# Optimization experiments

Measured on AMD Instinct MI355X. Metric: run time of the kernel, lower is better.

The kernel has to match this reference:

```python
import jax, jax.numpy as jnp
import numpy as np

NUM_HEADS = 12
NUM_PATCHES = 4096
DIM = 768
IN_DIMS = DIM // NUM_HEADS
SCALE = NUM_PATCHES ** (-0.5)
LN_EPS = 1e-5


def setup_inputs() -> dict:
    key = jax.random.key(0)
    ks = jax.random.split(key, 14)
    s = 0.02
    return {
        "x": jax.random.normal(ks[0], (16, NUM_PATCHES, DIM), dtype=jnp.float32),
        "wq": jax.random.normal(ks[1], (DIM, DIM), dtype=jnp.float32) * s,
        "bq": jnp.zeros((DIM,), dtype=jnp.float32),
        "wk": jax.random.normal(ks[2], (DIM, DIM), dtype=jnp.float32) * s,
        "bk": jnp.zeros((DIM,), dtype=jnp.float32),
        "w_g": jax.random.normal(ks[3], (NUM_PATCHES,), dtype=jnp.float32),
        "w_fc": jax.random.normal(ks[4], (IN_DIMS, DIM), dtype=jnp.float32) * s,
        "b_fc": jnp.zeros((DIM,), dtype=jnp.float32),
        "w_fc2": jax.random.normal(ks[5], (NUM_HEADS, NUM_HEADS), dtype=jnp.float32) * s,
        "b_fc2": jnp.zeros((NUM_HEADS,), dtype=jnp.float32),
        "w_proj": jax.random.normal(ks[6], (DIM, DIM), dtype=jnp.float32) * s,
        "b_proj": jnp.zeros((DIM,), dtype=jnp.float32),
        "gamma": jnp.ones((DIM,), dtype=jnp.float32),
        "beta": jnp.zeros((DIM,), dtype=jnp.float32),
    }


def layernorm(x, gamma, beta):
    mu = jnp.mean(x, axis=-1, keepdims=True)
    var = jnp.mean(jnp.square(x - mu), axis=-1, keepdims=True)
    return (x - mu) * jax.lax.rsqrt(var + LN_EPS) * gamma + beta


def reference(x, wq, bq, wk, bk, w_g, w_fc, b_fc, w_fc2, b_fc2, w_proj, b_proj, gamma, beta):
    bs, n, d = x.shape
    q = x @ wq + bq                      # (b,n,d)  fc_q
    k = x @ wk + bk                      # (b,n,d)  fc_k (reassigned x in torch)
    # query_weight = (q^T @ w_g)^T -> (b,1,d); softmax over channel dim
    qw = jnp.einsum("bnd,n->bd", q, w_g) * SCALE
    A = jax.nn.softmax(qw, axis=-1)      # (b,d)
    # G = sum_n(A * k): A is constant over n, so equals A * sum_n k
    G = A * jnp.sum(k, axis=1)           # (b,d)
    # sigmoid gating chain on pooled q
    dv = jnp.mean(q, axis=1)             # (b,d)   AdaptiveAvgPool over n
    dv = dv.reshape(bs, NUM_HEADS, IN_DIMS)
    dv = jax.nn.gelu(dv @ w_fc + b_fc, approximate=False)   # (b,H,d)
    dv = dv.reshape(bs, d, NUM_HEADS)    # reshape (not transpose), as in torch
    dv = dv @ w_fc2 + b_fc2              # (b,d,H)
    dv = jax.nn.sigmoid(jnp.mean(dv, axis=-1))               # (b,d)
    G = G * dv                           # (b,d)
    out = (G[:, None, :] * k) @ w_proj + b_proj + layernorm(k, gamma, beta)
    return out
```

## Files before the change

kernel.cpp:

```cpp
#include <hip/hip_runtime.h>
#include <hip/hip_bf16.h>
#include <math.h>

#define NB 16
#define NP 4096
#define DDIM 768
#define MTOT (NB*NP)
#define N1 1536
#define SCALEF 0.015625f
#define LNEPS 1e-5f

typedef __attribute__((ext_vector_type(8))) short bf16x8;
typedef __attribute__((ext_vector_type(4))) float f32x4;
typedef __attribute__((ext_vector_type(4))) unsigned int u32x4;
typedef unsigned short us;

__device__ __forceinline__ us f2b(float f){
  union { float f; unsigned int u; } v; v.f = f;
  unsigned int u = v.u;
  unsigned int r = (u + 0x7FFFu + ((u >> 16) & 1u)) >> 16;
  return (us)r;
}
__device__ __forceinline__ unsigned int pack2(float a, float b){
  return (unsigned int)f2b(a) | ((unsigned int)f2b(b) << 16);
}
__device__ __forceinline__ float b2f(us h){
  union { unsigned int u; float f; } v; v.u = ((unsigned int)h) << 16;
  return v.f;
}
__device__ __forceinline__ float b2f_lo(unsigned int u){
  union { unsigned int x; float f; } v; v.x = u << 16; return v.f;
}
__device__ __forceinline__ float b2f_hi(unsigned int u){
  union { unsigned int x; float f; } v; v.x = u & 0xFFFF0000u; return v.f;
}

typedef __attribute__((address_space(1))) const unsigned int gas_u32;
typedef __attribute__((address_space(3))) unsigned int las_u32;
__device__ __forceinline__ void gl2lds16(const void* g, void* l){
  __builtin_amdgcn_global_load_lds((gas_u32*)g, (las_u32*)l, 16, 0, 0);
}

__global__ __launch_bounds__(256) void convert_x(const float* __restrict__ x,
                                                 us* __restrict__ xb){
  size_t i = ((size_t)blockIdx.x * 256 + threadIdx.x) * 8;
  const float4* s = reinterpret_cast<const float4*>(x + i);
  float4 a = s[0], b = s[1];
  u32x4 w;
  w[0] = pack2(a.x, a.y); w[1] = pack2(a.z, a.w);
  w[2] = pack2(b.x, b.y); w[3] = pack2(b.z, b.w);
  *reinterpret_cast<u32x4*>(xb + i) = w;
}

__global__ __launch_bounds__(256) void prep_w(const float* __restrict__ wq,
                                              const float* __restrict__ wk,
                                              const float* __restrict__ wp,
                                              us* __restrict__ wt1,
                                              us* __restrict__ wt2){
  int idx = blockIdx.x * 256 + threadIdx.x;
  const int tot1 = N1 * DDIM;
  if (idx < tot1){
    int n = idx / DDIM, k = idx % DDIM;
    float v = (n < DDIM) ? wq[k * DDIM + n] : wk[k * DDIM + (n - DDIM)];
    wt1[idx] = f2b(v);
  }
  int idx2 = idx - tot1;
  if (idx2 >= 0 && idx2 < DDIM * DDIM){
    int n = idx2 / DDIM, k = idx2 % DDIM;
    wt2[idx2] = f2b(wp[k * DDIM + n]);
  }
}

__global__ __launch_bounds__(256) void prep_wb(const us* __restrict__ wt2,
                                               const float* __restrict__ g,
                                               us* __restrict__ wbuf){
  size_t idx = (size_t)blockIdx.x * 256 + threadIdx.x;
  int d = (int)(idx % DDIM);
  size_t nd = idx / DDIM;
  int n = (int)(nd % DDIM);
  int b = (int)(nd / DDIM);
  float v = b2f(wt2[n * DDIM + d]) * g[(size_t)b * DDIM + d];
  wbuf[idx] = f2b(v);
}

__global__ __launch_bounds__(256) void ln_reduce(const float* __restrict__ lnS,
                                                 const float* __restrict__ lnQ,
                                                 float2* __restrict__ rstats){
  int r = blockIdx.x * 256 + threadIdx.x;
  float s = lnS[r] + lnS[MTOT + r] + lnS[2*MTOT + r];
  float q = lnQ[r] + lnQ[MTOT + r] + lnQ[2*MTOT + r];
  float mu = s * (1.0f / DDIM);
  float var = q * (1.0f / DDIM) - mu * mu;
  rstats[r] = make_float2(mu, rsqrtf(var + LNEPS));
}

__device__ __forceinline__ void gemm256_core(const us* __restrict__ Ag,
                                             const us* __restrict__ Bg,
                                             us* lds, int t,
                                             f32x4 (&acc)[4][4][2]){
  us* ldsA = lds;
  us* ldsB = lds + 32768;
  const int wave = t >> 6, lane = t & 63;
  const int wr = wave >> 2, wc = wave & 3, lr = lane & 15, lh = lane >> 4;
  const int srow = t >> 3;
  const int scell = (t & 7) ^ ((t >> 3) & 7);
  const int key8 = lane & 7;

  auto stage_all = [&](int kt){
    int pb = (kt & 1) << 14;
    #pragma unroll
    for (int j = 0; j < 4; ++j){
      const us* sa = Ag + (size_t)(j*64 + srow) * DDIM + kt*64 + scell*8;
      gl2lds16(sa, ldsA + pb + j*4096 + (wave << 9));
    }
    #pragma unroll
    for (int j = 0; j < 4; ++j){
      const us* sb = Bg + (size_t)(j*64 + srow) * DDIM + kt*64 + scell*8;
      gl2lds16(sb, ldsB + pb + j*4096 + (wave << 9));
    }
  };

  stage_all(0);

  bf16x8 av[4][2], bv0[2][2], bv1[2][2];

  for (int kt = 0; kt < 12; ++kt){
    asm volatile("s_waitcnt vmcnt(0)" ::: "memory");
    __builtin_amdgcn_sched_barrier(0);
    __builtin_amdgcn_s_barrier();
    if (kt < 11) stage_all(kt + 1);

    const int pb = (kt & 1) << 14;
    const us* Ab = ldsA + pb;
    const us* Bb = ldsB + pb;

    #pragma unroll
    for (int fm = 0; fm < 4; ++fm){
      int ra = 0*128 + wr*64 + fm*16 + lr;
      #pragma unroll
      for (int kk = 0; kk < 2; ++kk)
        av[fm][kk] = *reinterpret_cast<const bf16x8*>(
            &Ab[ra*64 + ((((kk<<2)|lh) ^ key8) << 3)]);
    }
    #pragma unroll
    for (int fn = 0; fn < 2; ++fn){
      int rb0 = 0*128 + wc*32 + fn*16 + lr;
      int rb1 = 1*128 + wc*32 + fn*16 + lr;
      #pragma unroll
      for (int kk = 0; kk < 2; ++kk){
        bv0[fn][kk] = *reinterpret_cast<const bf16x8*>(
            &Bb[rb0*64 + ((((kk<<2)|lh) ^ key8) << 3)]);
        bv1[fn][kk] = *reinterpret_cast<const bf16x8*>(
            &Bb[rb1*64 + ((((kk<<2)|lh) ^ key8) << 3)]);
      }
    }
    #pragma unroll
    for (int fm = 0; fm < 4; ++fm)
      #pragma unroll
      for (int fn = 0; fn < 2; ++fn)
        #pragma unroll
        for (int kk = 0; kk < 2; ++kk){
          acc[0][fm][fn] = __builtin_amdgcn_mfma_f32_16x16x32_bf16(
              bv0[fn][kk], av[fm][kk], acc[0][fm][fn], 0, 0, 0);
          acc[1][fm][fn] = __builtin_amdgcn_mfma_f32_16x16x32_bf16(
              bv1[fn][kk], av[fm][kk], acc[1][fm][fn], 0, 0, 0);
        }

    #pragma unroll
    for (int fm = 0; fm < 4; ++fm){
      int ra = 1*128 + wr*64 + fm*16 + lr;
      #pragma unroll
      for (int kk = 0; kk < 2; ++kk)
        av[fm][kk] = *reinterpret_cast<const bf16x8*>(
            &Ab[ra*64 + ((((kk<<2)|lh) ^ key8) << 3)]);
    }
    #pragma unroll
    for (int fm = 0; fm < 4; ++fm)
      #pragma unroll
      for (int fn = 0; fn < 2; ++fn)
        #pragma unroll
        for (int kk = 0; kk < 2; ++kk){
          acc[2][fm][fn] = __builtin_amdgcn_mfma_f32_16x16x32_bf16(
              bv0[fn][kk], av[fm][kk], acc[2][fm][fn], 0, 0, 0);
          acc[3][fm][fn] = __builtin_amdgcn_mfma_f32_16x16x32_bf16(
              bv1[fn][kk], av[fm][kk], acc[3][fm][fn], 0, 0, 0);
        }
  }
  __builtin_amdgcn_s_barrier();
}

__global__ __launch_bounds__(512, 2) void gemm_qk(
    const us* __restrict__ xb, const us* __restrict__ wt1,
    const float* __restrict__ bq, const float* __restrict__ bk,
    const float* __restrict__ w_g,
    us* __restrict__ kout,
    float* __restrict__ qwp, float* __restrict__ qsp, float* __restrict__ ksp,
    float* __restrict__ lnS, float* __restrict__ lnQ)
{
  extern __shared__ us lds[];
  int bid = blockIdx.x;
  int swz = (bid & 7) * ((int)gridDim.x >> 3) + (bid >> 3);
  int bn = swz % 6, bm = swz / 6;
  int m0 = bm * 256, n0 = bn * 256;
  int t = threadIdx.x;

  f32x4 acc[4][4][2] = {};
  gemm256_core(xb + (size_t)m0 * DDIM, wt1 + (size_t)n0 * DDIM, lds, t, acc);

  int wave = t >> 6, lane = t & 63;
  int wr = wave >> 2, wc = wave & 3, lr = lane & 15, lh = lane >> 4;
  bool is_q = (n0 < DDIM);
  int b = m0 >> 12, mc = (m0 & (NP-1)) >> 8;

  float4 bias4[2][2];
  #pragma unroll
  for (int qn = 0; qn < 2; ++qn)
    #pragma unroll
    for (int fn = 0; fn < 2; ++fn){
      int col = qn*128 + wc*32 + fn*16 + lh*4;
      bias4[qn][fn] = *reinterpret_cast<const float4*>(
          is_q ? &bq[n0 + col] : &bk[n0 - DDIM + col]);
    }

  #pragma unroll
  for (int p = 0; p < 4; ++p){
    int qm = p >> 1, qn = p & 1;
    #pragma unroll
    for (int fm = 0; fm < 4; ++fm){
      int row = qm*128 + wr*64 + fm*16 + lr;
      #pragma unroll
      for (int fn = 0; fn < 2; ++fn){
        int col = qn*128 + wc*32 + fn*16 + lh*4;
        uint2 w;
        w.x = pack2(acc[p][fm][fn][0] + bias4[qn][fn].x,
                    acc[p][fm][fn][1] + bias4[qn][fn].y);
        w.y = pack2(acc[p][fm][fn][2] + bias4[qn][fn].z,
                    acc[p][fm][fn][3] + bias4[qn][fn].w);
        *reinterpret_cast<uint2*>(&lds[row*256 + (col ^ ((row & 7) << 3))]) = w;
      }
    }
  }
  __syncthreads();

  int c8 = t & 31, rb = t >> 5;
  float cp[8] = {0,0,0,0,0,0,0,0};
  float cpw[8] = {0,0,0,0,0,0,0,0};
  float rs16[16], rq16[16];
  #pragma unroll
  for (int s = 0; s < 16; ++s){
    int row = s*16 + rb;
    u32x4 ch = *reinterpret_cast<const u32x4*>(&lds[row*256 + ((c8 ^ (row & 7)) << 3)]);
    float v[8];
    #pragma unroll
    for (int i = 0; i < 4; ++i){ v[2*i] = b2f_lo(ch[i]); v[2*i+1] = b2f_hi(ch[i]); }
    if (is_q){
      float wg = w_g[(m0 & (NP-1)) + row];
      #pragma unroll
      for (int j = 0; j < 8; ++j){ cp[j] += v[j]; cpw[j] += wg * v[j]; }
    } else {
      *reinterpret_cast<u32x4*>(kout + (size_t)(m0+row)*DDIM + (n0 - DDIM) + c8*8) = ch;
      float ss = 0.f, qq = 0.f;
      #pragma unroll
      for (int j = 0; j < 8; ++j){ cp[j] += v[j]; ss += v[j]; qq += v[j]*v[j]; }
      rs16[s] = ss; rq16[s] = qq;
    }
  }
  __syncthreads();
  float* colP  = reinterpret_cast<float*>(lds);
  float* colPw = colP + 4096;
  float* rowP  = colP + 8192;
  float* rowQ  = colP + 16384;
  #pragma unroll
  for (int j = 0; j < 8; ++j){
    colP[(c8*8+j)*16 + rb] = cp[j];
    if (is_q) colPw[(c8*8+j)*16 + rb] = cpw[j];
  }
  if (!is_q){
    #pragma unroll
    for (int s = 0; s < 16; ++s){
      int row = s*16 + rb;
      rowP[row*32 + c8] = rs16[s];
      rowQ[row*32 + c8] = rq16[s];
    }
  }
  __syncthreads();
  if (t < 256){
    float s0 = 0.f;
    #pragma unroll
    for (int i = 0; i < 16; ++i) s0 += colP[t*16 + i];
    size_t base = ((size_t)b * 16 + mc) * DDIM;
    if (is_q){
      float s1 = 0.f;
      #pragma unroll
      for (int i = 0; i < 16; ++i) s1 += colPw[t*16 + i];
      qwp[base + n0 + t] = s1;
      qsp[base + n0 + t] = s0;
    } else {
      ksp[base + (n0 - DDIM) + t] = s0;
      float rs_ = 0.f, rq_ = 0.f;
      #pragma unroll
      for (int i = 0; i < 32; ++i){ rs_ += rowP[t*32 + i]; rq_ += rowQ[t*32 + i]; }
      int kb = bn - 3;
      lnS[(size_t)kb * MTOT + m0 + t] = rs_;
      lnQ[(size_t)kb * MTOT + m0 + t] = rq_;
    }
  }
}

__global__ __launch_bounds__(256) void combine(
    const float* __restrict__ qwp, const float* __restrict__ qsp, const float* __restrict__ ksp,
    const float* __restrict__ w_fc, const float* __restrict__ b_fc,
    const float* __restrict__ w_fc2, const float* __restrict__ b_fc2,
    float* __restrict__ g)
{
  __shared__ float smA[DDIM];
  __shared__ float smQM[DDIM];
  __shared__ float smKS[DDIM];
  __shared__ float tmat[12][DDIM];
  __shared__ float red[256];
  __shared__ float wbar[12];
  __shared__ float bbar;
  int b = blockIdx.x, t = threadIdx.x;

  for (int col = t; col < DDIM; col += 256){
    float s0 = 0.f, s1 = 0.f, s2 = 0.f;
    for (int mc = 0; mc < 16; ++mc){
      size_t base = ((size_t)b * 16 + mc) * DDIM + col;
      s0 += qwp[base]; s1 += qsp[base]; s2 += ksp[base];
    }
    smA[col] = s0 * SCALEF;
    smQM[col] = s1 * (1.0f / NP);
    smKS[col] = s2;
  }
  __syncthreads();
  float lmax = -1e30f;
  for (int col = t; col < DDIM; col += 256) lmax = fmaxf(lmax, smA[col]);
  red[t] = lmax; __syncthreads();
  for (int off = 128; off; off >>= 1){
    if (t < off) red[t] = fmaxf(red[t], red[t + off]);
    __syncthreads();
  }
  float mx = red[0];
  __syncthreads();
  float lsum = 0.f;
  for (int col = t; col < DDIM; col += 256){
    float e = __expf(smA[col] - mx);
    smA[col] = e; lsum += e;
  }
  red[t] = lsum; __syncthreads();
  for (int off = 128; off; off >>= 1){
    if (t < off) red[t] += red[t + off];
    __syncthreads();
  }
  float inv = 1.0f / red[0];
  for (int col = t; col < DDIM; col += 256) smA[col] *= inv;

  if (t < 12){
    float s = 0.f;
    for (int j = 0; j < 12; ++j) s += w_fc2[t * 12 + j];
    wbar[t] = s * (1.0f / 12.0f);
  }
  if (t == 12){
    float s = 0.f;
    for (int j = 0; j < 12; ++j) s += b_fc2[j];
    bbar = s * (1.0f / 12.0f);
  }
  __syncthreads();
  for (int idx = t; idx < 12 * DDIM; idx += 256){
    int h = idx / DDIM, j = idx % DDIM;
    float s = b_fc[j];
    const float* qm = &smQM[h * 64];
    #pragma unroll 4
    for (int i = 0; i < 64; ++i) s += qm[i] * w_fc[i * DDIM + j];
    tmat[h][j] = 0.5f * s * (1.0f + erff(s * 0.70710678118654752f));
  }
  __syncthreads();
  for (int p = t; p < DDIM; p += 256){
    float s = bbar;
    #pragma unroll
    for (int m = 0; m < 12; ++m){
      int f = p * 12 + m;
      s += tmat[f / DDIM][f % DDIM] * wbar[m];
    }
    float dv = 1.0f / (1.0f + __expf(-s));
    g[(size_t)b * DDIM + p] = smA[p] * smKS[p] * dv;
  }
}

__global__ __launch_bounds__(512, 2) void gemm_out(
    const us* __restrict__ kin, const us* __restrict__ wbuf,
    const float2* __restrict__ rstats,
    const float* __restrict__ bp, const float* __restrict__ gamma,
    const float* __restrict__ beta,
    float* __restrict__ out)
{
  extern __shared__ us lds[];
  int bid = blockIdx.x;
  int swz = (bid & 7) * ((int)gridDim.x >> 3) + (bid >> 3);
  int bn = swz % 3, bm = swz / 3;
  int m0 = bm * 256, n0 = bn * 256;
  int t = threadIdx.x;
  int b = m0 >> 12;

  f32x4 acc[4][4][2] = {};
  gemm256_core(kin + (size_t)m0 * DDIM,
               wbuf + (size_t)b * DDIM * DDIM + (size_t)n0 * DDIM, lds, t, acc);

  int wave = t >> 6, lane = t & 63;
  int wr = wave >> 2, wc = wave & 3, lr = lane & 15, lh = lane >> 4;

  #pragma unroll
  for (int j = 0; j < 16; ++j){
    int row = j*16 + (t >> 5);
    const us* src = kin + (size_t)(m0 + row) * DDIM + n0 + (((t & 31) ^ (row & 7)) << 3);
    gl2lds16(src, lds + j*4096 + (wave << 9));
  }
  float2 st2[2][4];
  #pragma unroll
  for (int qm = 0; qm < 2; ++qm)
    #pragma unroll
    for (int fm = 0; fm < 4; ++fm)
      st2[qm][fm] = rstats[m0 + qm*128 + wr*64 + fm*16 + lr];
  asm volatile("s_waitcnt vmcnt(0)" ::: "memory");
  __syncthreads();

  #pragma unroll
  for (int p = 0; p < 4; ++p){
    int qm = p >> 1, qn = p & 1;
    #pragma unroll
    for (int fn = 0; fn < 2; ++fn){
      int col = qn*128 + wc*32 + fn*16 + lh*4;
      float4 bpv = *reinterpret_cast<const float4*>(&bp[n0 + col]);
      float4 gmv = *reinterpret_cast<const float4*>(&gamma[n0 + col]);
      float4 btv = *reinterpret_cast<const float4*>(&beta[n0 + col]);
      #pragma unroll
      for (int fm = 0; fm < 4; ++fm){
        int row = qm*128 + wr*64 + fm*16 + lr;
        uint2 kw = *reinterpret_cast<const uint2*>(&lds[row*256 + (col ^ ((row & 7) << 3))]);
        float2 st = st2[qm][fm];
        acc[p][fm][fn][0] += bpv.x + (b2f_lo(kw.x) - st.x) * st.y * gmv.x + btv.x;
        acc[p][fm][fn][1] += bpv.y + (b2f_hi(kw.x) - st.x) * st.y * gmv.y + btv.y;
        acc[p][fm][fn][2] += bpv.z + (b2f_lo(kw.y) - st.x) * st.y * gmv.z + btv.z;
        acc[p][fm][fn][3] += bpv.w + (b2f_hi(kw.y) - st.x) * st.y * gmv.w + btv.w;
      }
    }
  }
  __syncthreads();

  float* fb = reinterpret_cast<float*>(lds);
  #pragma unroll
  for (int h = 0; h < 2; ++h){
    #pragma unroll
    for (int qm2 = 0; qm2 < 2; ++qm2){
      int p = qm2*2 + h;
      #pragma unroll
      for (int fm = 0; fm < 4; ++fm){
        int row = qm2*128 + wr*64 + fm*16 + lr;
        #pragma unroll
        for (int fn = 0; fn < 2; ++fn){
          int c = wc*32 + fn*16 + lh*4;
          *reinterpret_cast<f32x4*>(&fb[row*128 + (c ^ ((row & 7) << 2))]) = acc[p][fm][fn];
        }
      }
    }
    __syncthreads();
    #pragma unroll
    for (int s = 0; s < 16; ++s){
      int u = s*512 + t;
      int row = u >> 5, c4 = u & 31;
      float4 vv = *reinterpret_cast<const float4*>(&fb[row*128 + ((c4 ^ (row & 7)) << 2)]);
      *reinterpret_cast<float4*>(&out[(size_t)(m0 + row) * DDIM + n0 + h*128 + c4*4]) = vv;
    }
    __syncthreads();
  }
}

extern "C" void kernel_launch(void* const* d_in, const int* in_sizes, int n_in,
                              void* d_out, int out_size, void* d_ws, size_t ws_size,
                              hipStream_t stream)
{
  const float* x      = (const float*)d_in[0];
  const float* wq     = (const float*)d_in[1];
  const float* bq     = (const float*)d_in[2];
  const float* wk     = (const float*)d_in[3];
  const float* bk     = (const float*)d_in[4];
  const float* w_g    = (const float*)d_in[5];
  const float* w_fc   = (const float*)d_in[6];
  const float* b_fc   = (const float*)d_in[7];
  const float* w_fc2  = (const float*)d_in[8];
  const float* b_fc2  = (const float*)d_in[9];
  const float* w_proj = (const float*)d_in[10];
  const float* b_proj = (const float*)d_in[11];
  const float* gamma  = (const float*)d_in[12];
  const float* beta   = (const float*)d_in[13];
  float* out = (float*)d_out;

  char* ws = (char*)d_ws;
  us*     xb    = (us*)(ws);
  us*     kbuf  = (us*)(ws + 100663296);
  us*     wt1   = (us*)(ws + 201326592);
  us*     wt2   = (us*)(ws + 203685888);
  us*     wbuf  = (us*)(ws + 204865536);
  float*  qwp   = (float*)(ws + 223739904);
  float*  qsp   = (float*)(ws + 224526336);
  float*  ksp   = (float*)(ws + 225312768);
  float*  lnS   = (float*)(ws + 226099200);
  float*  lnQ   = (float*)(ws + 226885632);
  float*  g     = (float*)(ws + 227672064);
  float2* rstat = (float2*)(ws + 227721216);

  convert_x<<<dim3(MTOT * DDIM / (256 * 8)), dim3(256), 0, stream>>>(x, xb);
  prep_w<<<dim3((N1 * DDIM + DDIM * DDIM) / 256), dim3(256), 0, stream>>>(wq, wk, w_proj, wt1, wt2);
  gemm_qk<<<dim3((MTOT / 256) * (N1 / 256)), dim3(512), 131072, stream>>>(
      xb, wt1, bq, bk, w_g, kbuf, qwp, qsp, ksp, lnS, lnQ);
  ln_reduce<<<dim3(MTOT / 256), dim3(256), 0, stream>>>(lnS, lnQ, rstat);
  combine<<<dim3(NB), dim3(256), 0, stream>>>(qwp, qsp, ksp, w_fc, b_fc, w_fc2, b_fc2, g);
  prep_wb<<<dim3(NB * DDIM * DDIM / 256), dim3(256), 0, stream>>>(wt2, g, wbuf);
  gemm_out<<<dim3((MTOT / 256) * (DDIM / 256)), dim3(512), 131072, stream>>>(
      kbuf, wbuf, rstat, b_proj, gamma, beta, out);
}
```

Baseline: 515.1 us.

## Eliminate Q GEMM by reducing x first then multiplying reduced vectors by wq

Q is only needed through linear reductions over rows (the w_g-weighted sum and the mean), so the code now reduces x itself (weighted and plain column sums) and multiplies those per-batch vectors by wq in a small matrix-vector kernel. The big GEMM then computes only K, which halves its N dimension and its MFMA work. The K column sum is also taken from x sums times wk, and bias terms are folded in analytically inside combine. The cost is an extra pass over the bf16 x buffer plus two small kernels, and sums now come from bf16 x rather than from the bf16-rounded q and k.

```diff
diff --git a/kernel.cpp b/kernel.cpp
--- a/kernel.cpp
+++ b/kernel.cpp
@@ -6,7 +6,6 @@
 #define NP 4096
 #define DDIM 768
 #define MTOT (NB*NP)
-#define N1 1536
 #define SCALEF 0.015625f
 #define LNEPS 1e-5f
 
@@ -52,35 +51,94 @@
   *reinterpret_cast<u32x4*>(xb + i) = w;
 }
 
-__global__ __launch_bounds__(256) void prep_w(const float* __restrict__ wq,
-                                              const float* __restrict__ wk,
+__global__ __launch_bounds__(256) void prep_w(const float* __restrict__ wk,
                                               const float* __restrict__ wp,
-                                              us* __restrict__ wt1,
+                                              us* __restrict__ wtk,
                                               us* __restrict__ wt2){
   int idx = blockIdx.x * 256 + threadIdx.x;
-  const int tot1 = N1 * DDIM;
-  if (idx < tot1){
+  const int tot = DDIM * DDIM;
+  if (idx < tot){
     int n = idx / DDIM, k = idx % DDIM;
-    float v = (n < DDIM) ? wq[k * DDIM + n] : wk[k * DDIM + (n - DDIM)];
-    wt1[idx] = f2b(v);
-  }
-  int idx2 = idx - tot1;
-  if (idx2 >= 0 && idx2 < DDIM * DDIM){
-    int n = idx2 / DDIM, k = idx2 % DDIM;
-    wt2[idx2] = f2b(wp[k * DDIM + n]);
-  }
-}
-
-__global__ __launch_bounds__(256) void prep_wb(const us* __restrict__ wt2,
-                                               const float* __restrict__ g,
-                                               us* __restrict__ wbuf){
-  size_t idx = (size_t)blockIdx.x * 256 + threadIdx.x;
-  int d = (int)(idx % DDIM);
-  size_t nd = idx / DDIM;
-  int n = (int)(nd % DDIM);
-  int b = (int)(nd / DDIM);
-  float v = b2f(wt2[n * DDIM + d]) * g[(size_t)b * DDIM + d];
-  wbuf[idx] = f2b(v);
+    wtk[idx] = f2b(wk[k * DDIM + n]);
+  }
+  int i2 = idx - tot;
+  if (i2 >= 0 && i2 < tot){
+    int n = i2 / DDIM, k = i2 % DDIM;
+    wt2[i2] = f2b(wp[k * DDIM + n]);
+  }
+}
+
+__global__ __launch_bounds__(192) void xred(const us* __restrict__ xb,
+                                            const float* __restrict__ w_g,
+                                            float* __restrict__ xwp,
+                                            float* __restrict__ xsp){
+  __shared__ float sw[2][DDIM], ss[2][DDIM];
+  int blk = blockIdx.x, t = threadIdx.x;
+  int cg = (t % 96) * 8;
+  int h = t / 96;
+  int r0 = blk * 128;
+  float accw[8] = {0,0,0,0,0,0,0,0}, accs[8] = {0,0,0,0,0,0,0,0};
+  for (int r = h; r < 128; r += 2){
+    int row = r0 + r;
+    float wg = w_g[row & (NP - 1)];
+    bf16x8 v = *reinterpret_cast<const bf16x8*>(xb + (size_t)row * DDIM + cg);
+    #pragma unroll
+    for (int j = 0; j < 8; ++j){
+      float f = b2f((us)v[j]);
+      accs[j] += f; accw[j] += wg * f;
+    }
+  }
+  #pragma unroll
+  for (int j = 0; j < 8; ++j){ sw[h][cg + j] = accw[j]; ss[h][cg + j] = accs[j]; }
+  __syncthreads();
+  if (h == 0){
+    int b = r0 >> 12, mc = (r0 & (NP - 1)) >> 7;
+    size_t base = ((size_t)b * 32 + mc) * DDIM;
+    #pragma unroll
+    for (int j = 0; j < 8; ++j){
+      xwp[base + cg + j] = accw[j] + sw[1][cg + j];
+      xsp[base + cg + j] = accs[j] + ss[1][cg + j];
+    }
+  }
+}
+
+__global__ __launch_bounds__(256) void xmv(const float* __restrict__ xwp,
+                                           const float* __restrict__ xsp,
+                                           const float* __restrict__ wq,
+                                           const float* __restrict__ wk,
+                                           float* __restrict__ qwv,
+                                           float* __restrict__ qmv,
+                                           float* __restrict__ ksv){
+  __shared__ float sxw[DDIM], sxs[DDIM];
+  __shared__ float pa[2][128], pb_[2][128], pc[2][128];
+  int blk = blockIdx.x;
+  int b = blk / 6, dc = (blk % 6) * 128;
+  int t = threadIdx.x;
+  for (int col = t; col < DDIM; col += 256){
+    float s0 = 0.f, s1 = 0.f;
+    for (int mc = 0; mc < 32; ++mc){
+      size_t base = ((size_t)b * 32 + mc) * DDIM + col;
+      s0 += xwp[base]; s1 += xsp[base];
+    }
+    sxw[col] = s0; sxs[col] = s1;
+  }
+  __syncthreads();
+  int d = dc + (t & 127), h = t >> 7;
+  float aq = 0.f, am = 0.f, ak = 0.f;
+  for (int k = h * 384; k < h * 384 + 384; ++k){
+    float w1 = wq[(size_t)k * DDIM + d];
+    float w2 = wk[(size_t)k * DDIM + d];
+    float xw = sxw[k], xs = sxs[k];
+    aq += xw * w1; am += xs * w1; ak += xs * w2;
+  }
+  pa[h][t & 127] = aq; pb_[h][t & 127] = am; pc[h][t & 127] = ak;
+  __syncthreads();
+  if (h == 0){
+    size_t o = (size_t)b * DDIM + d;
+    qwv[o] = aq + pa[1][t];
+    qmv[o] = am + pb_[1][t];
+    ksv[o] = ak + pc[1][t];
+  }
 }
 
 __global__ __launch_bounds__(256) void ln_reduce(const float* __restrict__ lnS,
@@ -189,28 +247,24 @@
   __builtin_amdgcn_s_barrier();
 }
 
-__global__ __launch_bounds__(512, 2) void gemm_qk(
-    const us* __restrict__ xb, const us* __restrict__ wt1,
-    const float* __restrict__ bq, const float* __restrict__ bk,
-    const float* __restrict__ w_g,
+__global__ __launch_bounds__(512, 2) void gemm_k(
+    const us* __restrict__ xb, const us* __restrict__ wtk,
+    const float* __restrict__ bk,
     us* __restrict__ kout,
-    float* __restrict__ qwp, float* __restrict__ qsp, float* __restrict__ ksp,
     float* __restrict__ lnS, float* __restrict__ lnQ)
 {
   extern __shared__ us lds[];
   int bid = blockIdx.x;
   int swz = (bid & 7) * ((int)gridDim.x >> 3) + (bid >> 3);
-  int bn = swz % 6, bm = swz / 6;
+  int bn = swz % 3, bm = swz / 3;
   int m0 = bm * 256, n0 = bn * 256;
   int t = threadIdx.x;
 
   f32x4 acc[4][4][2] = {};
-  gemm256_core(xb + (size_t)m0 * DDIM, wt1 + (size_t)n0 * DDIM, lds, t, acc);
+  gemm256_core(xb + (size_t)m0 * DDIM, wtk + (size_t)n0 * DDIM, lds, t, acc);
 
   int wave = t >> 6, lane = t & 63;
   int wr = wave >> 2, wc = wave & 3, lr = lane & 15, lh = lane >> 4;
-  bool is_q = (n0 < DDIM);
-  int b = m0 >> 12, mc = (m0 & (NP-1)) >> 8;
 
   float4 bias4[2][2];
   #pragma unroll
@@ -218,8 +272,7 @@
     #pragma unroll
     for (int fn = 0; fn < 2; ++fn){
       int col = qn*128 + wc*32 + fn*16 + lh*4;
-      bias4[qn][fn] = *reinterpret_cast<const float4*>(
-          is_q ? &bq[n0 + col] : &bk[n0 - DDIM + col]);
+      bias4[qn][fn] = *reinterpret_cast<const float4*>(&bk[n0 + col]);
     }
 
   #pragma unroll
@@ -243,72 +296,56 @@
   __syncthreads();
 
   int c8 = t & 31, rb = t >> 5;
-  float cp[8] = {0,0,0,0,0,0,0,0};
-  float cpw[8] = {0,0,0,0,0,0,0,0};
   float rs16[16], rq16[16];
   #pragma unroll
   for (int s = 0; s < 16; ++s){
     int row = s*16 + rb;
     u32x4 ch = *reinterpret_cast<const u32x4*>(&lds[row*256 + ((c8 ^ (row & 7)) << 3)]);
-    float v[8];
-    #pragma unroll
-    for (int i = 0; i < 4; ++i){ v[2*i] = b2f_lo(ch[i]); v[2*i+1] = b2f_hi(ch[i]); }
-    if (is_q){
-      float wg = w_g[(m0 & (NP-1)) + row];
-      #pragma unroll
-      for (int j = 0; j < 8; ++j){ cp[j] += v[j]; cpw[j] += wg * v[j]; }
-    } else {
-      *reinterpret_cast<u32x4*>(kout + (size_t)(m0+row)*DDIM + (n0 - DDIM) + c8*8) = ch;
-      float ss = 0.f, qq = 0.f;
-      #pragma unroll
-      for (int j = 0; j < 8; ++j){ cp[j] += v[j]; ss += v[j]; qq += v[j]*v[j]; }
-      rs16[s] = ss; rq16[s] = qq;
-    }
-  }
-  __syncthreads();
-  float* colP  = reinterpret_cast<float*>(lds);
-  float* colPw = colP + 4096;
-  float* rowP  = colP + 8192;
-  float* rowQ  = colP + 16384;
-  #pragma unroll
-  for (int j = 0; j < 8; ++j){
-    colP[(c8*8+j)*16 + rb] = cp[j];
-    if (is_q) colPw[(c8*8+j)*16 + rb] = cpw[j];
-  }
-  if (!is_q){
-    #pragma unroll
-    for (int s = 0; s < 16; ++s){
-      int row = s*16 + rb;
-      rowP[row*32 + c8] = rs16[s];
-      rowQ[row*32 + c8] = rq16[s];
-    }
+    *reinterpret_cast<u32x4*>(kout + (size_t)(m0+row)*DDIM + n0 + c8*8) = ch;
+    float ss = 0.f, qq = 0.f;
+    #pragma unroll
+    for (int i = 0; i < 4; ++i){
+      float v0 = b2f_lo(ch[i]), v1 = b2f_hi(ch[i]);
+      ss += v0 + v1; qq += v0*v0 + v1*v1;
+    }
+    rs16[s] = ss; rq16[s] = qq;
+  }
+  __syncthreads();
+  float* rowP = reinterpret_cast<float*>(lds);
+  float* rowQ = rowP + 8192;
+  #pragma unroll
+  for (int s = 0; s < 16; ++s){
+    int row = s*16 + rb;
+    rowP[row*32 + c8] = rs16[s];
+    rowQ[row*32 + c8] = rq16[s];
   }
   __syncthreads();
   if (t < 256){
-    float s0 = 0.f;
-    #pragma unroll
-    for (int i = 0; i < 16; ++i) s0 += colP[t*16 + i];
-    size_t base = ((size_t)b * 16 + mc) * DDIM;
-    if (is_q){
-      float s1 = 0.f;
-      #pragma unroll
-      for (int i = 0; i < 16; ++i) s1 += colPw[t*16 + i];
-      qwp[base + n0 + t] = s1;
-      qsp[base + n0 + t] = s0;
-    } else {
-      ksp[base + (n0 - DDIM) + t] = s0;
-      float rs_ = 0.f, rq_ = 0.f;
-      #pragma unroll
-      for (int i = 0; i < 32; ++i){ rs_ += rowP[t*32 + i]; rq_ += rowQ[t*32 + i]; }
-      int kb = bn - 3;
-      lnS[(size_t)kb * MTOT + m0 + t] = rs_;
-      lnQ[(size_t)kb * MTOT + m0 + t] = rq_;
-    }
-  }
+    float rs_ = 0.f, rq_ = 0.f;
+    #pragma unroll
+    for (int i = 0; i < 32; ++i){ rs_ += rowP[t*32 + i]; rq_ += rowQ[t*32 + i]; }
+    lnS[(size_t)bn * MTOT + m0 + t] = rs_;
+    lnQ[(size_t)bn * MTOT + m0 + t] = rq_;
+  }
+}
+
+__global__ __launch_bounds__(256) void prep_wb(const us* __restrict__ wt2,
+                                               const float* __restrict__ g,
+                                               us* __restrict__ wbuf){
+  size_t idx = (size_t)blockIdx.x * 256 + threadIdx.x;
+  int d = (int)(idx % DDIM);
+  size_t nd = idx / DDIM;
+  int n = (int)(nd % DDIM);
+  int b = (int)(nd / DDIM);
+  float v = b2f(wt2[n * DDIM + d]) * g[(size_t)b * DDIM + d];
+  wbuf[idx] = f2b(v);
 }
 
 __global__ __launch_bounds__(256) void combine(
-    const float* __restrict__ qwp, const float* __restrict__ qsp, const float* __restrict__ ksp,
+    const float* __restrict__ qwv, const float* __restrict__ qmv,
+    const float* __restrict__ ksv,
+    const float* __restrict__ bq, const float* __restrict__ bk,
+    const float* __restrict__ w_g,
     const float* __restrict__ w_fc, const float* __restrict__ b_fc,
     const float* __restrict__ w_fc2, const float* __restrict__ b_fc2,
     float* __restrict__ g)
@@ -322,17 +359,24 @@
   __shared__ float bbar;
   int b = blockIdx.x, t = threadIdx.x;
 
+  float sw = 0.f;
+  for (int i = t; i < NP; i += 256) sw += w_g[i];
+  red[t] = sw; __syncthreads();
+  for (int off = 128; off; off >>= 1){
+    if (t < off) red[t] += red[t + off];
+    __syncthreads();
+  }
+  float sumwg = red[0];
+  __syncthreads();
+
   for (int col = t; col < DDIM; col += 256){
-    float s0 = 0.f, s1 = 0.f, s2 = 0.f;
-    for (int mc = 0; mc < 16; ++mc){
-      size_t base = ((size_t)b * 16 + mc) * DDIM + col;
-      s0 += qwp[base]; s1 += qsp[base]; s2 += ksp[base];
-    }
-    smA[col] = s0 * SCALEF;
-    smQM[col] = s1 * (1.0f / NP);
-    smKS[col] = s2;
-  }
-  __syncthreads();
+    size_t o = (size_t)b * DDIM + col;
+    smA[col]  = (qwv[o] + bq[col] * sumwg) * SCALEF;
+    smQM[col] = qmv[o] * (1.0f / NP) + bq[col];
+    smKS[col] = ksv[o] + (float)NP * bk[col];
+  }
+  __syncthreads();
+
   float lmax = -1e30f;
   for (int col = t; col < DDIM; col += 256) lmax = fmaxf(lmax, smA[col]);
   red[t] = lmax; __syncthreads();
@@ -498,24 +542,29 @@
   char* ws = (char*)d_ws;
   us*     xb    = (us*)(ws);
   us*     kbuf  = (us*)(ws + 100663296);
-  us*     wt1   = (us*)(ws + 201326592);
-  us*     wt2   = (us*)(ws + 203685888);
-  us*     wbuf  = (us*)(ws + 204865536);
-  float*  qwp   = (float*)(ws + 223739904);
-  float*  qsp   = (float*)(ws + 224526336);
-  float*  ksp   = (float*)(ws + 225312768);
-  float*  lnS   = (float*)(ws + 226099200);
-  float*  lnQ   = (float*)(ws + 226885632);
-  float*  g     = (float*)(ws + 227672064);
-  float2* rstat = (float2*)(ws + 227721216);
+  us*     wtk   = (us*)(ws + 201326592);
+  us*     wt2   = (us*)(ws + 202506240);
+  us*     wbuf  = (us*)(ws + 203685888);
+  float*  xwp   = (float*)(ws + 222560256);
+  float*  xsp   = (float*)(ws + 224133120);
+  float*  lnS   = (float*)(ws + 225705984);
+  float*  lnQ   = (float*)(ws + 226492416);
+  float*  g     = (float*)(ws + 227278848);
+  float2* rstat = (float2*)(ws + 227328000);
+  float*  qwv   = (float*)(ws + 227852288);
+  float*  qmv   = (float*)(ws + 227901440);
+  float*  ksv   = (float*)(ws + 227950592);
 
   convert_x<<<dim3(MTOT * DDIM / (256 * 8)), dim3(256), 0, stream>>>(x, xb);
-  prep_w<<<dim3((N1 * DDIM + DDIM * DDIM) / 256), dim3(256), 0, stream>>>(wq, wk, w_proj, wt1, wt2);
-  gemm_qk<<<dim3((MTOT / 256) * (N1 / 256)), dim3(512), 131072, stream>>>(
-      xb, wt1, bq, bk, w_g, kbuf, qwp, qsp, ksp, lnS, lnQ);
+  prep_w<<<dim3(2 * DDIM * DDIM / 256), dim3(256), 0, stream>>>(wk, w_proj, wtk, wt2);
+  xred<<<dim3(MTOT / 128), dim3(192), 0, stream>>>(xb, w_g, xwp, xsp);
+  xmv<<<dim3(NB * 6), dim3(256), 0, stream>>>(xwp, xsp, wq, wk, qwv, qmv, ksv);
+  gemm_k<<<dim3((MTOT / 256) * 3), dim3(512), 131072, stream>>>(
+      xb, wtk, bk, kbuf, lnS, lnQ);
   ln_reduce<<<dim3(MTOT / 256), dim3(256), 0, stream>>>(lnS, lnQ, rstat);
-  combine<<<dim3(NB), dim3(256), 0, stream>>>(qwp, qsp, ksp, w_fc, b_fc, w_fc2, b_fc2, g);
+  combine<<<dim3(NB), dim3(256), 0, stream>>>(
+      qwv, qmv, ksv, bq, bk, w_g, w_fc, b_fc, w_fc2, b_fc2, g);
   prep_wb<<<dim3(NB * DDIM * DDIM / 256), dim3(256), 0, stream>>>(wt2, g, wbuf);
-  gemm_out<<<dim3((MTOT / 256) * (DDIM / 256)), dim3(512), 131072, stream>>>(
+  gemm_out<<<dim3((MTOT / 256) * 3), dim3(512), 131072, stream>>>(
       kbuf, wbuf, rstat, b_proj, gamma, beta, out);
 }
```

New measurement: 513.7 us. No clear change (-0.3%).
